# Performance work log

Hardware: AMD Instinct MI355X
Metric: run time of the kernel (lower is better)

Reference implementation:

```python
import jax, jax.numpy as jnp
import numpy as np

EPS = 1e-5

def conv1x1(x, w, b):
    # x: [B,C,H,W], w: [O,C], b: [O]
    return jnp.einsum('bchw,oc->bohw', x, w) + b[None, :, None, None]

def bn_eval(x, w, b, m, v):
    inv = w / jnp.sqrt(v + EPS)
    return (x - m[None, :, None, None]) * inv[None, :, None, None] + b[None, :, None, None]

def setup_inputs() -> dict:
    key = jax.random.key(0)
    ks = jax.random.split(key, 32)
    B, Fg, Fl, Fi, H, W = 4, 128, 128, 64, 64, 64
    d = {}
    d['g'] = jax.random.normal(ks[0], (B, Fg, H, W), jnp.float32)
    d['x'] = jax.random.normal(ks[1], (B, Fl, H, W), jnp.float32)
    d['wg_w'] = jax.random.normal(ks[2], (Fi, Fg), jnp.float32) * 0.1
    d['wg_b'] = jax.random.normal(ks[3], (Fi,), jnp.float32) * 0.1
    d['bng_w'] = jax.random.uniform(ks[4], (Fi,), jnp.float32)
    d['bng_b'] = jax.random.normal(ks[5], (Fi,), jnp.float32) * 0.1
    d['bng_m'] = jax.random.normal(ks[6], (Fi,), jnp.float32) * 0.1
    d['bng_v'] = jax.random.uniform(ks[7], (Fi,), jnp.float32) + 0.5
    d['wx_w'] = jax.random.normal(ks[8], (Fi, Fl), jnp.float32) * 0.1
    d['wx_b'] = jax.random.normal(ks[9], (Fi,), jnp.float32) * 0.1
    d['bnx_w'] = jax.random.uniform(ks[10], (Fi,), jnp.float32)
    d['bnx_b'] = jax.random.normal(ks[11], (Fi,), jnp.float32) * 0.1
    d['bnx_m'] = jax.random.normal(ks[12], (Fi,), jnp.float32) * 0.1
    d['bnx_v'] = jax.random.uniform(ks[13], (Fi,), jnp.float32) + 0.5
    d['q_w'] = jax.random.normal(ks[14], (Fi // 8, Fi), jnp.float32) * 0.1
    d['q_b'] = jax.random.normal(ks[15], (Fi // 8,), jnp.float32) * 0.1
    d['k_w'] = jax.random.normal(ks[16], (Fi // 8, Fi), jnp.float32) * 0.1
    d['k_b'] = jax.random.normal(ks[17], (Fi // 8,), jnp.float32) * 0.1
    d['v_w'] = jax.random.normal(ks[18], (Fi, Fi), jnp.float32) * 0.1
    d['v_b'] = jax.random.normal(ks[19], (Fi,), jnp.float32) * 0.1
    d['sa_gamma'] = jax.random.normal(ks[20], (1,), jnp.float32)
    d['psi_w'] = jax.random.normal(ks[21], (1, Fi), jnp.float32) * 0.1
    d['psi_b'] = jax.random.normal(ks[22], (1,), jnp.float32) * 0.1
    d['bnp_w'] = jax.random.uniform(ks[23], (1,), jnp.float32)
    d['bnp_b'] = jax.random.normal(ks[24], (1,), jnp.float32) * 0.1
    d['bnp_m'] = jax.random.normal(ks[25], (1,), jnp.float32) * 0.1
    d['bnp_v'] = jax.random.uniform(ks[26], (1,), jnp.float32) + 0.5
    return d

def reference(g, x, wg_w, wg_b, bng_w, bng_b, bng_m, bng_v,
              wx_w, wx_b, bnx_w, bnx_b, bnx_m, bnx_v,
              q_w, q_b, k_w, k_b, v_w, v_b, sa_gamma,
              psi_w, psi_b, bnp_w, bnp_b, bnp_m, bnp_v):
    g1 = bn_eval(conv1x1(g, wg_w, wg_b), bng_w, bng_b, bng_m, bng_v)
    x1 = bn_eval(conv1x1(x, wx_w, wx_b), bnx_w, bnx_b, bnx_m, bnx_v)
    c = jax.nn.relu(g1 + x1)  # [B, Fi, H, W]
    B, C, H, W = c.shape
    N = H * W
    q = conv1x1(c, q_w, q_b).reshape(B, -1, N)  # [B, Fi/8, N]
    k = conv1x1(c, k_w, k_b).reshape(B, -1, N)
    v = conv1x1(c, v_w, v_b).reshape(B, C, N)
    energy = jnp.einsum('bcn,bcm->bnm', q, k)    # [B, N, N]
    attn = jax.nn.softmax(energy, axis=-1)
    sa_out = jnp.einsum('bcm,bnm->bcn', v, attn).reshape(B, C, H, W)
    attended = sa_gamma[0] * sa_out + c
    psi = jax.nn.sigmoid(bn_eval(conv1x1(attended, psi_w, psi_b), bnp_w, bnp_b, bnp_m, bnp_v))
    return x * psi
```

## Files before the change

### kernel.cpp

```cpp
#include <hip/hip_runtime.h>
#include <hip/hip_bf16.h>


typedef short bf16x8 __attribute__((ext_vector_type(8)));
typedef unsigned short u16x8 __attribute__((ext_vector_type(8)));
typedef unsigned short u16x4 __attribute__((ext_vector_type(4)));
typedef float f32x4 __attribute__((ext_vector_type(4)));

__device__ __forceinline__ unsigned short f2b(float f) {
  unsigned u = __builtin_bit_cast(unsigned, f);
  u = (u + 0x7FFFu + ((u >> 16) & 1u)) >> 16;
  return (unsigned short)u;
}

#define EPSV 1e-5f

#define WCAT_OFF   0u
#define WQKV_OFF   32768u
#define BIASC_OFF  44032u
#define BIASQ_OFF  44288u
#define PSIW_OFF   44608u
#define SCAL_OFF   44864u
#define C_OFF      45056u
#define Q_OFF      (C_OFF + 4194304u)
#define K_OFF      (Q_OFF + 262144u)
#define V_OFF      (K_OFF + 262144u)
#define OPART_OFF  (V_OFF + 2097152u)
#define ML_OFF     (OPART_OFF + 16777216u)

__global__ __launch_bounds__(256) void prep_kernel(
    const float* __restrict__ wg_w, const float* __restrict__ wg_b,
    const float* __restrict__ bng_w, const float* __restrict__ bng_b,
    const float* __restrict__ bng_m, const float* __restrict__ bng_v,
    const float* __restrict__ wx_w, const float* __restrict__ wx_b,
    const float* __restrict__ bnx_w, const float* __restrict__ bnx_b,
    const float* __restrict__ bnx_m, const float* __restrict__ bnx_v,
    const float* __restrict__ q_w, const float* __restrict__ q_b,
    const float* __restrict__ k_w, const float* __restrict__ k_b,
    const float* __restrict__ v_w, const float* __restrict__ v_b,
    const float* __restrict__ psi_w, const float* __restrict__ psi_b,
    const float* __restrict__ bnp_w, const float* __restrict__ bnp_b,
    const float* __restrict__ bnp_m, const float* __restrict__ bnp_v,
    const float* __restrict__ sa_gamma,
    unsigned short* __restrict__ Wcat, unsigned short* __restrict__ Wqkv,
    float* __restrict__ bias_c, float* __restrict__ bias_q,
    float* __restrict__ psi_w2, float* __restrict__ scal)
{
  const int t = threadIdx.x;
  const int bid = blockIdx.x;
  if (bid < 16) {
    int o = bid * 4 + (t >> 6);
    int k = (t & 63) * 4;
    float inv;
    const float* src;
    if (k < 128) {
      inv = bng_w[o] * rsqrtf(bng_v[o] + EPSV);
      src = wg_w + o * 128 + k;
    } else {
      inv = bnx_w[o] * rsqrtf(bnx_v[o] + EPSV);
      src = wx_w + o * 128 + (k - 128);
    }
    float4 wv = *(const float4*)src;
    u16x4 pk;
    pk[0] = f2b(wv.x * inv); pk[1] = f2b(wv.y * inv);
    pk[2] = f2b(wv.z * inv); pk[3] = f2b(wv.w * inv);
    *(u16x4*)(Wcat + o * 256 + k) = pk;
    return;
  }
  for (int idx = t; idx < 80 * 64; idx += 256) {
    int r = idx >> 6, k = idx & 63;
    float wv;
    if (r < 8)       wv = q_w[r * 64 + k];
    else if (r < 16) wv = k_w[(r - 8) * 64 + k];
    else             wv = v_w[(r - 16) * 64 + k];
    Wqkv[idx] = f2b(wv);
  }
  if (t < 64) {
    int o = t;
    float invg = bng_w[o] * rsqrtf(bng_v[o] + EPSV);
    float invx = bnx_w[o] * rsqrtf(bnx_v[o] + EPSV);
    bias_c[o] = (wg_b[o] - bng_m[o]) * invg + bng_b[o]
              + (wx_b[o] - bnx_m[o]) * invx + bnx_b[o];
    float invp = bnp_w[0] * rsqrtf(bnp_v[0] + EPSV);
    psi_w2[o] = psi_w[o] * invp;
  }
  if (t < 80)
    bias_q[t] = (t < 8) ? q_b[t] : (t < 16 ? k_b[t - 8] : v_b[t - 16]);
  if (t == 0) {
    float invp = bnp_w[0] * rsqrtf(bnp_v[0] + EPSV);
    scal[0] = sa_gamma[0];
    scal[1] = (psi_b[0] - bnp_m[0]) * invp + bnp_b[0];
  }
}

__global__ __launch_bounds__(256) void conv_qkv_kernel(
    const float* __restrict__ g, const float* __restrict__ x,
    const unsigned short* __restrict__ Wcat, const unsigned short* __restrict__ Wqkv,
    const float* __restrict__ bias_c, const float* __restrict__ bias_q,
    float* __restrict__ c_out, unsigned short* __restrict__ Qb,
    unsigned short* __restrict__ Kb, unsigned short* __restrict__ Vb)
{
  __shared__ __attribute__((aligned(16))) unsigned short xt[32][264];
  __shared__ __attribute__((aligned(16))) unsigned short clds[32][72];

  const int t = threadIdx.x;
  const int bid = blockIdx.x;
  const int b = bid >> 7;
  const int n0 = (bid & 127) << 5;

  {
    const int col4 = t & 7;
    const int rowg = t >> 3;
    float4 v[8];
    #pragma unroll
    for (int rr = 0; rr < 8; ++rr) {
      int row = rowg * 8 + rr;
      const float* src = (row < 128)
          ? (g + ((size_t)(b * 128 + row)) * 4096 + n0 + col4 * 4)
          : (x + ((size_t)(b * 128 + (row - 128))) * 4096 + n0 + col4 * 4);
      v[rr] = *(const float4*)src;
    }
    #pragma unroll
    for (int j = 0; j < 4; ++j) {
      u16x8 pk;
      #pragma unroll
      for (int rr = 0; rr < 8; ++rr)
        pk[rr] = f2b(((const float*)&v[rr])[j]);
      *(u16x8*)(&xt[col4 * 4 + j][rowg * 8]) = pk;
    }
  }
  __syncthreads();

  const int l = t & 63, w = t >> 6;
  const int l15 = l & 15, lg = l >> 4;
  f32x4 zf = {0.f, 0.f, 0.f, 0.f};

  f32x4 acc[2];
  acc[0] = acc[1] = zf;
  const int orow = w * 16 + l15;
  #pragma unroll
  for (int ks = 0; ks < 8; ++ks) {
    bf16x8 af = *(const bf16x8*)(Wcat + orow * 256 + ks * 32 + lg * 8);
    #pragma unroll
    for (int ns = 0; ns < 2; ++ns) {
      bf16x8 bfv = *(const bf16x8*)(&xt[ns * 16 + l15][ks * 32 + lg * 8]);
      acc[ns] = __builtin_amdgcn_mfma_f32_16x16x32_bf16(af, bfv, acc[ns], 0, 0, 0);
    }
  }
  #pragma unroll
  for (int r = 0; r < 4; ++r) {
    int o = w * 16 + lg * 4 + r;
    float bc = bias_c[o];
    #pragma unroll
    for (int ns = 0; ns < 2; ++ns) {
      float cv = fmaxf(acc[ns][r] + bc, 0.f);
      int n = ns * 16 + l15;
      c_out[((size_t)(b * 64 + o)) * 4096 + n0 + n] = cv;
      clds[n][o] = f2b(cv);
    }
  }
  __syncthreads();

  #pragma unroll
  for (int i = 0; i < 3; ++i) {
    int tau = w + 4 * i;
    if (tau >= 10) break;
    int t5 = tau % 5, ns = tau / 5;
    f32x4 a2 = zf;
    #pragma unroll
    for (int kk = 0; kk < 2; ++kk) {
      bf16x8 af = *(const bf16x8*)(Wqkv + (t5 * 16 + l15) * 64 + kk * 32 + lg * 8);
      bf16x8 bfv = *(const bf16x8*)(&clds[ns * 16 + l15][kk * 32 + lg * 8]);
      a2 = __builtin_amdgcn_mfma_f32_16x16x32_bf16(af, bfv, a2, 0, 0, 0);
    }
    #pragma unroll
    for (int r = 0; r < 4; ++r) {
      int row = t5 * 16 + lg * 4 + r;
      int ngl = n0 + ns * 16 + l15;
      float val = a2[r] + bias_q[row];
      if (t5 == 0) {
        if (row < 8) Qb[(((size_t)b << 12) + ngl) * 8 + row] = f2b(val);
        else         Kb[(((size_t)b << 12) + ngl) * 8 + (row - 8)] = f2b(val);
      } else {
        int vch = (t5 - 1) * 16 + lg * 4 + r;
        Vb[((size_t)(b * 64 + vch)) * 4096 + ngl] = f2b(val);
      }
    }
  }
}

__global__ __launch_bounds__(256) void attn_partial_kernel(
    const unsigned short* __restrict__ Qb, const unsigned short* __restrict__ Kb,
    const unsigned short* __restrict__ Vb,
    float* __restrict__ Opart, float* __restrict__ ml)
{
  __shared__ __attribute__((aligned(16))) unsigned short klds[64][8];
  __shared__ __attribute__((aligned(16))) unsigned short vlds[64][72];
  __shared__ __attribute__((aligned(16))) unsigned short plds[4][16][72];

  const int t = threadIdx.x;
  const int bid = blockIdx.x;
  const int qt = bid & 63;
  const int b = (bid >> 6) & 3;
  const int ci = bid >> 8;
  const int n0 = qt << 6;
  const int l = t & 63, w = t >> 6;
  const int l15 = l & 15, lg = l >> 4;

  bf16x8 qf = {0, 0, 0, 0, 0, 0, 0, 0};
  if (lg == 0)
    qf = *(const bf16x8*)(Qb + (((size_t)b << 12) + n0 + w * 16 + l15) * 8);

  f32x4 zf = {0.f, 0.f, 0.f, 0.f};
  f32x4 O[4];
  O[0] = O[1] = O[2] = O[3] = zf;
  float m_run[4] = {-INFINITY, -INFINITY, -INFINITY, -INFINITY};
  float l_run[4] = {0.f, 0.f, 0.f, 0.f};

  const int m_lo = ci << 10, m_hi = (ci + 1) << 10;
  for (int m0 = m_lo; m0 < m_hi; m0 += 64) {
    if (t < 64)
      *(int4*)(&klds[t][0]) = *(const int4*)(Kb + (((size_t)b << 12) + m0 + t) * 8);
    #pragma unroll
    for (int i = 0; i < 2; ++i) {
      int ci2 = t + 256 * i;
      int row = ci2 >> 3, off = ci2 & 7;
      *(int4*)(&vlds[row][off * 8]) =
          *(const int4*)(Vb + ((size_t)(b * 64 + row)) * 4096 + m0 + off * 8);
    }
    __syncthreads();

    f32x4 e[4];
    #pragma unroll
    for (int mt = 0; mt < 4; ++mt) {
      bf16x8 kf = *(const bf16x8*)(&klds[mt * 16 + l15][0]);
      e[mt] = __builtin_amdgcn_mfma_f32_16x16x32_bf16(qf, kf, zf, 0, 0, 0);
    }

    #pragma unroll
    for (int r = 0; r < 4; ++r) {
      float vm = fmaxf(fmaxf(e[0][r], e[1][r]), fmaxf(e[2][r], e[3][r]));
      vm = fmaxf(vm, __shfl_xor(vm, 1));
      vm = fmaxf(vm, __shfl_xor(vm, 2));
      vm = fmaxf(vm, __shfl_xor(vm, 4));
      vm = fmaxf(vm, __shfl_xor(vm, 8));
      float nm = fmaxf(m_run[r], vm);
      float sc = __expf(m_run[r] - nm);
      float s = 0.f;
      #pragma unroll
      for (int mt = 0; mt < 4; ++mt) {
        float p = __expf(e[mt][r] - nm);
        e[mt][r] = p;
        s += p;
      }
      s += __shfl_xor(s, 1);
      s += __shfl_xor(s, 2);
      s += __shfl_xor(s, 4);
      s += __shfl_xor(s, 8);
      l_run[r] = l_run[r] * sc + s;
      m_run[r] = nm;
      #pragma unroll
      for (int mt = 0; mt < 4; ++mt)
        plds[w][lg * 4 + r][mt * 16 + l15] = f2b(e[mt][r]);
      #pragma unroll
      for (int ct = 0; ct < 4; ++ct) O[ct][r] *= sc;
    }

    #pragma unroll
    for (int ct = 0; ct < 4; ++ct) {
      #pragma unroll
      for (int kk = 0; kk < 2; ++kk) {
        bf16x8 pa = *(const bf16x8*)(&plds[w][l15][kk * 32 + lg * 8]);
        bf16x8 vb = *(const bf16x8*)(&vlds[ct * 16 + l15][kk * 32 + lg * 8]);
        O[ct] = __builtin_amdgcn_mfma_f32_16x16x32_bf16(pa, vb, O[ct], 0, 0, 0);
      }
    }
    __syncthreads();
  }

  const size_t pb = ((size_t)(ci * 4 + b)) << 12;
  #pragma unroll
  for (int ct = 0; ct < 4; ++ct) {
    int ch = ct * 16 + l15;
    #pragma unroll
    for (int r = 0; r < 4; ++r) {
      int qg = n0 + w * 16 + lg * 4 + r;
      Opart[(pb + qg) * 64 + ch] = O[ct][r];
    }
  }
  if (l15 == 0) {
    #pragma unroll
    for (int r = 0; r < 4; ++r) {
      int qg = n0 + w * 16 + lg * 4 + r;
      float2 mv;
      mv.x = m_run[r]; mv.y = l_run[r];
      *(float2*)(ml + (pb + qg) * 2) = mv;
    }
  }
}

__global__ __launch_bounds__(256) void combine_kernel(
    const float* __restrict__ Opart, const float* __restrict__ ml,
    const float* __restrict__ c_in, const float* __restrict__ xin,
    const float* __restrict__ psi_w2, const float* __restrict__ scal,
    float* __restrict__ out)
{
  __shared__ __attribute__((aligned(16))) float c_lds[64][68];
  __shared__ float psi_lds[64];

  const int t = threadIdx.x;
  const int bid = blockIdx.x;
  const int b = bid >> 6;
  const int n0 = (bid & 63) << 6;

  #pragma unroll
  for (int i = 0; i < 4; ++i) {
    int idx = t + 256 * i;
    int ch = idx >> 4, c4 = idx & 15;
    float4 cv = *(const float4*)(c_in + ((size_t)(b * 64 + ch)) * 4096 + n0 + c4 * 4);
    *(float4*)(&c_lds[ch][c4 * 4]) = cv;
  }
  __syncthreads();

  const int q = t >> 2, cg = t & 3;
  const int qg = n0 + q;

  float m[4], li[4];
  float M = -INFINITY;
  #pragma unroll
  for (int ci = 0; ci < 4; ++ci) {
    float2 v = *(const float2*)(ml + ((((size_t)(ci * 4 + b)) << 12) + qg) * 2);
    m[ci] = v.x; li[ci] = v.y;
    M = fmaxf(M, v.x);
  }
  float L = 0.f, wgt[4];
  #pragma unroll
  for (int ci = 0; ci < 4; ++ci) {
    wgt[ci] = __expf(m[ci] - M);
    L += wgt[ci] * li[ci];
  }
  float4 o4[4];
  o4[0] = o4[1] = o4[2] = o4[3] = make_float4(0.f, 0.f, 0.f, 0.f);
  #pragma unroll
  for (int ci = 0; ci < 4; ++ci) {
    const float* base = Opart + ((((size_t)(ci * 4 + b)) << 12) + qg) * 64 + cg * 16;
    float wv = wgt[ci];
    #pragma unroll
    for (int k = 0; k < 4; ++k) {
      float4 p = *(const float4*)(base + k * 4);
      o4[k].x += wv * p.x; o4[k].y += wv * p.y;
      o4[k].z += wv * p.z; o4[k].w += wv * p.w;
    }
  }
  const float invL = 1.f / L;
  const float gamma = scal[0], psi_c = scal[1];
  float ps = 0.f;
  #pragma unroll
  for (int k = 0; k < 4; ++k) {
    const float* op = (const float*)&o4[k];
    #pragma unroll
    for (int jj = 0; jj < 4; ++jj) {
      int ch = cg * 16 + k * 4 + jj;
      ps += psi_w2[ch] * (gamma * (op[jj] * invL) + c_lds[ch][q]);
    }
  }
  ps += __shfl_xor(ps, 1);
  ps += __shfl_xor(ps, 2);
  if (cg == 0)
    psi_lds[q] = 1.f / (1.f + __expf(-(ps + psi_c)));
  __syncthreads();

  #pragma unroll
  for (int i = 0; i < 8; ++i) {
    int idx = t + 256 * i;
    int f = idx >> 4, c4 = idx & 15;
    size_t off = ((size_t)(b * 128 + f)) * 4096 + n0 + c4 * 4;
    float4 xv = *(const float4*)(xin + off);
    float4 ov;
    ov.x = xv.x * psi_lds[c4 * 4 + 0];
    ov.y = xv.y * psi_lds[c4 * 4 + 1];
    ov.z = xv.z * psi_lds[c4 * 4 + 2];
    ov.w = xv.w * psi_lds[c4 * 4 + 3];
    *(float4*)(out + off) = ov;
  }
}

extern "C" void kernel_launch(void* const* d_in, const int* in_sizes, int n_in,
                              void* d_out, int out_size, void* d_ws, size_t ws_size,
                              hipStream_t stream) {
  (void)in_sizes; (void)n_in; (void)out_size; (void)ws_size;
  const float* g     = (const float*)d_in[0];
  const float* x     = (const float*)d_in[1];
  const float* wg_w  = (const float*)d_in[2];
  const float* wg_b  = (const float*)d_in[3];
  const float* bng_w = (const float*)d_in[4];
  const float* bng_b = (const float*)d_in[5];
  const float* bng_m = (const float*)d_in[6];
  const float* bng_v = (const float*)d_in[7];
  const float* wx_w  = (const float*)d_in[8];
  const float* wx_b  = (const float*)d_in[9];
  const float* bnx_w = (const float*)d_in[10];
  const float* bnx_b = (const float*)d_in[11];
  const float* bnx_m = (const float*)d_in[12];
  const float* bnx_v = (const float*)d_in[13];
  const float* q_w   = (const float*)d_in[14];
  const float* q_b   = (const float*)d_in[15];
  const float* k_w   = (const float*)d_in[16];
  const float* k_b   = (const float*)d_in[17];
  const float* v_w   = (const float*)d_in[18];
  const float* v_b   = (const float*)d_in[19];
  const float* sa_g  = (const float*)d_in[20];
  const float* psi_w = (const float*)d_in[21];
  const float* psi_b = (const float*)d_in[22];
  const float* bnp_w = (const float*)d_in[23];
  const float* bnp_b = (const float*)d_in[24];
  const float* bnp_m = (const float*)d_in[25];
  const float* bnp_v = (const float*)d_in[26];
  float* out = (float*)d_out;

  char* ws = (char*)d_ws;
  unsigned short* Wcat = (unsigned short*)(ws + WCAT_OFF);
  unsigned short* Wqkv = (unsigned short*)(ws + WQKV_OFF);
  float* bias_c = (float*)(ws + BIASC_OFF);
  float* bias_q = (float*)(ws + BIASQ_OFF);
  float* psiw2  = (float*)(ws + PSIW_OFF);
  float* scal   = (float*)(ws + SCAL_OFF);
  float* c_buf  = (float*)(ws + C_OFF);
  unsigned short* Qb = (unsigned short*)(ws + Q_OFF);
  unsigned short* Kb = (unsigned short*)(ws + K_OFF);
  unsigned short* Vb = (unsigned short*)(ws + V_OFF);
  float* Opart = (float*)(ws + OPART_OFF);
  float* mlb   = (float*)(ws + ML_OFF);

  hipLaunchKernelGGL(prep_kernel, dim3(17), dim3(256), 0, stream,
                     wg_w, wg_b, bng_w, bng_b, bng_m, bng_v,
                     wx_w, wx_b, bnx_w, bnx_b, bnx_m, bnx_v,
                     q_w, q_b, k_w, k_b, v_w, v_b,
                     psi_w, psi_b, bnp_w, bnp_b, bnp_m, bnp_v, sa_g,
                     Wcat, Wqkv, bias_c, bias_q, psiw2, scal);

  hipLaunchKernelGGL(conv_qkv_kernel, dim3(512), dim3(256), 0, stream,
                     g, x, Wcat, Wqkv, bias_c, bias_q, c_buf, Qb, Kb, Vb);

  hipLaunchKernelGGL(attn_partial_kernel, dim3(1024), dim3(256), 0, stream,
                     Qb, Kb, Vb, Opart, mlb);

  hipLaunchKernelGGL(combine_kernel, dim3(256), dim3(256), 0, stream,
                     Opart, mlb, c_buf, x, psiw2, scal, out);
}
```

Measured before the change: 188.9 us.

## Fuse prep into conv kernel and combine into attention via last-block counter

Weight folding (BN scale and bias) moves into the conv kernel, so the prep launch goes away. The combine step moves into the attention kernel: the last of 8 key-split blocks per query tile, found with an atomic counter, does the reduction. The key dimension is split 8 ways instead of 4, giving twice as many blocks. The c buffer and the O partials are stored in bf16 instead of fp32, and V is staged through LDS so it can be written with coalesced stores. This cuts launch count and memory traffic, at the cost of redundant per-block weight conversion, lower intermediate precision, and a counter reset that relies on the previous kernel's ordering.

```diff
diff --git a/kernel.cpp b/kernel.cpp
--- a/kernel.cpp
+++ b/kernel.cpp
@@ -7,28 +7,25 @@
 typedef unsigned short u16x4 __attribute__((ext_vector_type(4)));
 typedef float f32x4 __attribute__((ext_vector_type(4)));
 
-__device__ __forceinline__ unsigned short f2b(float f) {
-  unsigned u = __builtin_bit_cast(unsigned, f);
-  u = (u + 0x7FFFu + ((u >> 16) & 1u)) >> 16;
-  return (unsigned short)u;
+__device__ __forceinline__ unsigned short f2b16(float f) {
+  return __builtin_bit_cast(unsigned short, __float2bfloat16(f));
 }
+__device__ __forceinline__ float b2f(unsigned short u) {
+  return __bfloat162float(__builtin_bit_cast(__hip_bfloat16, u));
+}
 
 #define EPSV 1e-5f
 
-#define WCAT_OFF   0u
-#define WQKV_OFF   32768u
-#define BIASC_OFF  44032u
-#define BIASQ_OFF  44288u
-#define PSIW_OFF   44608u
-#define SCAL_OFF   44864u
-#define C_OFF      45056u
-#define Q_OFF      (C_OFF + 4194304u)
+#define C_OFF      0u
+#define Q_OFF      (C_OFF + 2097152u)
 #define K_OFF      (Q_OFF + 262144u)
 #define V_OFF      (K_OFF + 262144u)
 #define OPART_OFF  (V_OFF + 2097152u)
 #define ML_OFF     (OPART_OFF + 16777216u)
-
-__global__ __launch_bounds__(256) void prep_kernel(
+#define CNT_OFF    (ML_OFF + 1048576u)
+
+__global__ __launch_bounds__(256) void conv_fused_kernel(
+    const float* __restrict__ g, const float* __restrict__ x,
     const float* __restrict__ wg_w, const float* __restrict__ wg_b,
     const float* __restrict__ bng_w, const float* __restrict__ bng_b,
     const float* __restrict__ bng_m, const float* __restrict__ bng_v,
@@ -38,75 +35,20 @@
     const float* __restrict__ q_w, const float* __restrict__ q_b,
     const float* __restrict__ k_w, const float* __restrict__ k_b,
     const float* __restrict__ v_w, const float* __restrict__ v_b,
-    const float* __restrict__ psi_w, const float* __restrict__ psi_b,
-    const float* __restrict__ bnp_w, const float* __restrict__ bnp_b,
-    const float* __restrict__ bnp_m, const float* __restrict__ bnp_v,
-    const float* __restrict__ sa_gamma,
-    unsigned short* __restrict__ Wcat, unsigned short* __restrict__ Wqkv,
-    float* __restrict__ bias_c, float* __restrict__ bias_q,
-    float* __restrict__ psi_w2, float* __restrict__ scal)
-{
-  const int t = threadIdx.x;
-  const int bid = blockIdx.x;
-  if (bid < 16) {
-    int o = bid * 4 + (t >> 6);
-    int k = (t & 63) * 4;
-    float inv;
-    const float* src;
-    if (k < 128) {
-      inv = bng_w[o] * rsqrtf(bng_v[o] + EPSV);
-      src = wg_w + o * 128 + k;
-    } else {
-      inv = bnx_w[o] * rsqrtf(bnx_v[o] + EPSV);
-      src = wx_w + o * 128 + (k - 128);
-    }
-    float4 wv = *(const float4*)src;
-    u16x4 pk;
-    pk[0] = f2b(wv.x * inv); pk[1] = f2b(wv.y * inv);
-    pk[2] = f2b(wv.z * inv); pk[3] = f2b(wv.w * inv);
-    *(u16x4*)(Wcat + o * 256 + k) = pk;
-    return;
-  }
-  for (int idx = t; idx < 80 * 64; idx += 256) {
-    int r = idx >> 6, k = idx & 63;
-    float wv;
-    if (r < 8)       wv = q_w[r * 64 + k];
-    else if (r < 16) wv = k_w[(r - 8) * 64 + k];
-    else             wv = v_w[(r - 16) * 64 + k];
-    Wqkv[idx] = f2b(wv);
-  }
-  if (t < 64) {
-    int o = t;
-    float invg = bng_w[o] * rsqrtf(bng_v[o] + EPSV);
-    float invx = bnx_w[o] * rsqrtf(bnx_v[o] + EPSV);
-    bias_c[o] = (wg_b[o] - bng_m[o]) * invg + bng_b[o]
-              + (wx_b[o] - bnx_m[o]) * invx + bnx_b[o];
-    float invp = bnp_w[0] * rsqrtf(bnp_v[0] + EPSV);
-    psi_w2[o] = psi_w[o] * invp;
-  }
-  if (t < 80)
-    bias_q[t] = (t < 8) ? q_b[t] : (t < 16 ? k_b[t - 8] : v_b[t - 16]);
-  if (t == 0) {
-    float invp = bnp_w[0] * rsqrtf(bnp_v[0] + EPSV);
-    scal[0] = sa_gamma[0];
-    scal[1] = (psi_b[0] - bnp_m[0]) * invp + bnp_b[0];
-  }
-}
-
-__global__ __launch_bounds__(256) void conv_qkv_kernel(
-    const float* __restrict__ g, const float* __restrict__ x,
-    const unsigned short* __restrict__ Wcat, const unsigned short* __restrict__ Wqkv,
-    const float* __restrict__ bias_c, const float* __restrict__ bias_q,
-    float* __restrict__ c_out, unsigned short* __restrict__ Qb,
-    unsigned short* __restrict__ Kb, unsigned short* __restrict__ Vb)
+    unsigned short* __restrict__ cb, unsigned short* __restrict__ Qb,
+    unsigned short* __restrict__ Kb, unsigned short* __restrict__ Vb,
+    int* __restrict__ cnt)
 {
   __shared__ __attribute__((aligned(16))) unsigned short xt[32][264];
   __shared__ __attribute__((aligned(16))) unsigned short clds[32][72];
+  __shared__ __attribute__((aligned(16))) unsigned short vstage[64][36];
 
   const int t = threadIdx.x;
   const int bid = blockIdx.x;
   const int b = bid >> 7;
   const int n0 = (bid & 127) << 5;
+
+  if (bid == 0) cnt[t] = 0;
 
   {
     const int col4 = t & 7;
@@ -125,38 +67,60 @@
       u16x8 pk;
       #pragma unroll
       for (int rr = 0; rr < 8; ++rr)
-        pk[rr] = f2b(((const float*)&v[rr])[j]);
+        pk[rr] = f2b16(((const float*)&v[rr])[j]);
       *(u16x8*)(&xt[col4 * 4 + j][rowg * 8]) = pk;
     }
   }
-  __syncthreads();
 
   const int l = t & 63, w = t >> 6;
   const int l15 = l & 15, lg = l >> 4;
   f32x4 zf = {0.f, 0.f, 0.f, 0.f};
 
+  const int orow = w * 16 + l15;
+  const float invg = bng_w[orow] * rsqrtf(bng_v[orow] + EPSV);
+  const float invx = bnx_w[orow] * rsqrtf(bnx_v[orow] + EPSV);
+  bf16x8 afrag[8];
+  #pragma unroll
+  for (int ks = 0; ks < 8; ++ks) {
+    int k = ks * 32 + lg * 8;
+    const float* wp;
+    float sc;
+    if (k < 128) { wp = wg_w + orow * 128 + k;        sc = invg; }
+    else         { wp = wx_w + orow * 128 + (k - 128); sc = invx; }
+    float4 w0 = *(const float4*)wp;
+    float4 w1 = *(const float4*)(wp + 4);
+    u16x8 pk;
+    pk[0] = f2b16(w0.x * sc); pk[1] = f2b16(w0.y * sc);
+    pk[2] = f2b16(w0.z * sc); pk[3] = f2b16(w0.w * sc);
+    pk[4] = f2b16(w1.x * sc); pk[5] = f2b16(w1.y * sc);
+    pk[6] = f2b16(w1.z * sc); pk[7] = f2b16(w1.w * sc);
+    afrag[ks] = __builtin_bit_cast(bf16x8, pk);
+  }
+  __syncthreads();
+
   f32x4 acc[2];
   acc[0] = acc[1] = zf;
-  const int orow = w * 16 + l15;
   #pragma unroll
   for (int ks = 0; ks < 8; ++ks) {
-    bf16x8 af = *(const bf16x8*)(Wcat + orow * 256 + ks * 32 + lg * 8);
     #pragma unroll
     for (int ns = 0; ns < 2; ++ns) {
       bf16x8 bfv = *(const bf16x8*)(&xt[ns * 16 + l15][ks * 32 + lg * 8]);
-      acc[ns] = __builtin_amdgcn_mfma_f32_16x16x32_bf16(af, bfv, acc[ns], 0, 0, 0);
+      acc[ns] = __builtin_amdgcn_mfma_f32_16x16x32_bf16(afrag[ks], bfv, acc[ns], 0, 0, 0);
     }
   }
   #pragma unroll
   for (int r = 0; r < 4; ++r) {
     int o = w * 16 + lg * 4 + r;
-    float bc = bias_c[o];
+    float ig = bng_w[o] * rsqrtf(bng_v[o] + EPSV);
+    float ix = bnx_w[o] * rsqrtf(bnx_v[o] + EPSV);
+    float bc = (wg_b[o] - bng_m[o]) * ig + bng_b[o]
+             + (wx_b[o] - bnx_m[o]) * ix + bnx_b[o];
     #pragma unroll
     for (int ns = 0; ns < 2; ++ns) {
       float cv = fmaxf(acc[ns][r] + bc, 0.f);
-      int n = ns * 16 + l15;
-      c_out[((size_t)(b * 64 + o)) * 4096 + n0 + n] = cv;
-      clds[n][o] = f2b(cv);
+      unsigned short cv16 = f2b16(cv);
+      cb[((size_t)(b * 64 + o)) * 4096 + n0 + ns * 16 + l15] = cv16;
+      clds[ns * 16 + l15][o] = cv16;
     }
   }
   __syncthreads();
@@ -166,37 +130,75 @@
     int tau = w + 4 * i;
     if (tau >= 10) break;
     int t5 = tau % 5, ns = tau / 5;
+    int wrow = t5 * 16 + l15;
     f32x4 a2 = zf;
     #pragma unroll
     for (int kk = 0; kk < 2; ++kk) {
-      bf16x8 af = *(const bf16x8*)(Wqkv + (t5 * 16 + l15) * 64 + kk * 32 + lg * 8);
-      bf16x8 bfv = *(const bf16x8*)(&clds[ns * 16 + l15][kk * 32 + lg * 8]);
-      a2 = __builtin_amdgcn_mfma_f32_16x16x32_bf16(af, bfv, a2, 0, 0, 0);
-    }
-    #pragma unroll
-    for (int r = 0; r < 4; ++r) {
-      int row = t5 * 16 + lg * 4 + r;
-      int ngl = n0 + ns * 16 + l15;
-      float val = a2[r] + bias_q[row];
-      if (t5 == 0) {
-        if (row < 8) Qb[(((size_t)b << 12) + ngl) * 8 + row] = f2b(val);
-        else         Kb[(((size_t)b << 12) + ngl) * 8 + (row - 8)] = f2b(val);
-      } else {
+      int k = kk * 32 + lg * 8;
+      const float* wp = (wrow < 8)  ? (q_w + wrow * 64 + k)
+                      : (wrow < 16) ? (k_w + (wrow - 8) * 64 + k)
+                                    : (v_w + (wrow - 16) * 64 + k);
+      float4 w0 = *(const float4*)wp;
+      float4 w1 = *(const float4*)(wp + 4);
+      u16x8 pk;
+      pk[0] = f2b16(w0.x); pk[1] = f2b16(w0.y);
+      pk[2] = f2b16(w0.z); pk[3] = f2b16(w0.w);
+      pk[4] = f2b16(w1.x); pk[5] = f2b16(w1.y);
+      pk[6] = f2b16(w1.z); pk[7] = f2b16(w1.w);
+      bf16x8 bfv = *(const bf16x8*)(&clds[ns * 16 + l15][k]);
+      a2 = __builtin_amdgcn_mfma_f32_16x16x32_bf16(
+          __builtin_bit_cast(bf16x8, pk), bfv, a2, 0, 0, 0);
+    }
+    int ngl = n0 + ns * 16 + l15;
+    if (t5 == 0) {
+      u16x4 pk;
+      #pragma unroll
+      for (int r = 0; r < 4; ++r) {
+        int row = lg * 4 + r;
+        float bq = (row < 8) ? q_b[row] : k_b[row - 8];
+        pk[r] = f2b16(a2[r] + bq);
+      }
+      if (lg < 2)
+        *(u16x4*)(Qb + (((size_t)b << 12) + ngl) * 8 + lg * 4) = pk;
+      else
+        *(u16x4*)(Kb + (((size_t)b << 12) + ngl) * 8 + (lg - 2) * 4) = pk;
+    } else {
+      #pragma unroll
+      for (int r = 0; r < 4; ++r) {
         int vch = (t5 - 1) * 16 + lg * 4 + r;
-        Vb[((size_t)(b * 64 + vch)) * 4096 + ngl] = f2b(val);
+        vstage[vch][ns * 16 + l15] = f2b16(a2[r] + v_b[vch]);
       }
     }
   }
+  __syncthreads();
+
+  #pragma unroll
+  for (int i = 0; i < 2; ++i) {
+    int idx = t + 256 * i;
+    int row = idx >> 3, seg = idx & 7;
+    u16x4 pv = *(const u16x4*)(&vstage[row][seg * 4]);
+    *(u16x4*)(Vb + ((size_t)(b * 64 + row)) * 4096 + n0 + seg * 4) = pv;
+  }
 }
 
-__global__ __launch_bounds__(256) void attn_partial_kernel(
+__global__ __launch_bounds__(256) void attn_fused_kernel(
     const unsigned short* __restrict__ Qb, const unsigned short* __restrict__ Kb,
-    const unsigned short* __restrict__ Vb,
-    float* __restrict__ Opart, float* __restrict__ ml)
+    const unsigned short* __restrict__ Vb, const unsigned short* __restrict__ cb,
+    const float* __restrict__ xin,
+    const float* __restrict__ psi_w, const float* __restrict__ psi_b,
+    const float* __restrict__ bnp_w, const float* __restrict__ bnp_b,
+    const float* __restrict__ bnp_m, const float* __restrict__ bnp_v,
+    const float* __restrict__ sa_gamma,
+    unsigned short* __restrict__ Opart, float* __restrict__ ml,
+    int* __restrict__ cnt, float* __restrict__ out)
 {
-  __shared__ __attribute__((aligned(16))) unsigned short klds[64][8];
-  __shared__ __attribute__((aligned(16))) unsigned short vlds[64][72];
-  __shared__ __attribute__((aligned(16))) unsigned short plds[4][16][72];
+  __shared__ __attribute__((aligned(16))) char smem[19456];
+  __shared__ int is_last;
+  auto klds = (unsigned short(*)[8])smem;
+  auto vlds = (unsigned short(*)[72])(smem + 1024);
+  auto plds = (unsigned short(*)[16][72])(smem + 10240);
+  auto ml_lds = (float2(*)[8])smem;
+  float* psi_lds = (float*)(smem + 4096);
 
   const int t = threadIdx.x;
   const int bid = blockIdx.x;
@@ -217,7 +219,7 @@
   float m_run[4] = {-INFINITY, -INFINITY, -INFINITY, -INFINITY};
   float l_run[4] = {0.f, 0.f, 0.f, 0.f};
 
-  const int m_lo = ci << 10, m_hi = (ci + 1) << 10;
+  const int m_lo = ci << 9, m_hi = (ci + 1) << 9;
   for (int m0 = m_lo; m0 < m_hi; m0 += 64) {
     if (t < 64)
       *(int4*)(&klds[t][0]) = *(const int4*)(Kb + (((size_t)b << 12) + m0 + t) * 8);
@@ -261,7 +263,7 @@
       m_run[r] = nm;
       #pragma unroll
       for (int mt = 0; mt < 4; ++mt)
-        plds[w][lg * 4 + r][mt * 16 + l15] = f2b(e[mt][r]);
+        plds[w][lg * 4 + r][mt * 16 + l15] = f2b16(e[mt][r]);
       #pragma unroll
       for (int ct = 0; ct < 4; ++ct) O[ct][r] *= sc;
     }
@@ -285,7 +287,7 @@
     #pragma unroll
     for (int r = 0; r < 4; ++r) {
       int qg = n0 + w * 16 + lg * 4 + r;
-      Opart[(pb + qg) * 64 + ch] = O[ct][r];
+      Opart[(pb + qg) * 64 + ch] = f2b16(O[ct][r]);
     }
   }
   if (l15 == 0) {
@@ -297,72 +299,61 @@
       *(float2*)(ml + (pb + qg) * 2) = mv;
     }
   }
-}
-
-__global__ __launch_bounds__(256) void combine_kernel(
-    const float* __restrict__ Opart, const float* __restrict__ ml,
-    const float* __restrict__ c_in, const float* __restrict__ xin,
-    const float* __restrict__ psi_w2, const float* __restrict__ scal,
-    float* __restrict__ out)
-{
-  __shared__ __attribute__((aligned(16))) float c_lds[64][68];
-  __shared__ float psi_lds[64];
-
-  const int t = threadIdx.x;
-  const int bid = blockIdx.x;
-  const int b = bid >> 6;
-  const int n0 = (bid & 63) << 6;
-
-  #pragma unroll
-  for (int i = 0; i < 4; ++i) {
+
+  __threadfence();
+  __syncthreads();
+  if (t == 0)
+    is_last = (atomicAdd(&cnt[b * 64 + qt], 1) == 7);
+  __syncthreads();
+  if (!is_last) return;
+  __threadfence();
+
+  #pragma unroll
+  for (int i = 0; i < 2; ++i) {
     int idx = t + 256 * i;
-    int ch = idx >> 4, c4 = idx & 15;
-    float4 cv = *(const float4*)(c_in + ((size_t)(b * 64 + ch)) * 4096 + n0 + c4 * 4);
-    *(float4*)(&c_lds[ch][c4 * 4]) = cv;
-  }
-  __syncthreads();
+    int cj = idx >> 6, q = idx & 63;
+    ml_lds[q][cj] = *(const float2*)(ml + ((((size_t)(cj * 4 + b)) << 12) + n0 + q) * 2);
+  }
+  __syncthreads();
+
+  const float invp = bnp_w[0] * rsqrtf(bnp_v[0] + EPSV);
+  const float psi_c = (psi_b[0] - bnp_m[0]) * invp + bnp_b[0];
+  const float gamma = sa_gamma[0];
 
   const int q = t >> 2, cg = t & 3;
   const int qg = n0 + q;
 
-  float m[4], li[4];
   float M = -INFINITY;
   #pragma unroll
-  for (int ci = 0; ci < 4; ++ci) {
-    float2 v = *(const float2*)(ml + ((((size_t)(ci * 4 + b)) << 12) + qg) * 2);
-    m[ci] = v.x; li[ci] = v.y;
-    M = fmaxf(M, v.x);
-  }
-  float L = 0.f, wgt[4];
-  #pragma unroll
-  for (int ci = 0; ci < 4; ++ci) {
-    wgt[ci] = __expf(m[ci] - M);
-    L += wgt[ci] * li[ci];
-  }
-  float4 o4[4];
-  o4[0] = o4[1] = o4[2] = o4[3] = make_float4(0.f, 0.f, 0.f, 0.f);
-  #pragma unroll
-  for (int ci = 0; ci < 4; ++ci) {
-    const float* base = Opart + ((((size_t)(ci * 4 + b)) << 12) + qg) * 64 + cg * 16;
-    float wv = wgt[ci];
-    #pragma unroll
-    for (int k = 0; k < 4; ++k) {
-      float4 p = *(const float4*)(base + k * 4);
-      o4[k].x += wv * p.x; o4[k].y += wv * p.y;
-      o4[k].z += wv * p.z; o4[k].w += wv * p.w;
+  for (int cj = 0; cj < 8; ++cj) M = fmaxf(M, ml_lds[q][cj].x);
+  float L = 0.f, wgt[8];
+  #pragma unroll
+  for (int cj = 0; cj < 8; ++cj) {
+    wgt[cj] = __expf(ml_lds[q][cj].x - M);
+    L += wgt[cj] * ml_lds[q][cj].y;
+  }
+  float osum[16];
+  #pragma unroll
+  for (int k = 0; k < 16; ++k) osum[k] = 0.f;
+  #pragma unroll
+  for (int cj = 0; cj < 8; ++cj) {
+    const unsigned short* base =
+        Opart + ((((size_t)(cj * 4 + b)) << 12) + qg) * 64 + cg * 16;
+    float wv = wgt[cj];
+    #pragma unroll
+    for (int s4 = 0; s4 < 4; ++s4) {
+      u16x4 p = *(const u16x4*)(base + s4 * 4);
+      #pragma unroll
+      for (int j = 0; j < 4; ++j) osum[s4 * 4 + j] += wv * b2f(p[j]);
     }
   }
   const float invL = 1.f / L;
-  const float gamma = scal[0], psi_c = scal[1];
   float ps = 0.f;
   #pragma unroll
-  for (int k = 0; k < 4; ++k) {
-    const float* op = (const float*)&o4[k];
-    #pragma unroll
-    for (int jj = 0; jj < 4; ++jj) {
-      int ch = cg * 16 + k * 4 + jj;
-      ps += psi_w2[ch] * (gamma * (op[jj] * invL) + c_lds[ch][q]);
-    }
+  for (int k = 0; k < 16; ++k) {
+    int ch = cg * 16 + k;
+    float cv = b2f(cb[((size_t)(b * 64 + ch)) * 4096 + qg]);
+    ps += (psi_w[ch] * invp) * (gamma * (osum[k] * invL) + cv);
   }
   ps += __shfl_xor(ps, 1);
   ps += __shfl_xor(ps, 2);
@@ -419,32 +410,22 @@
   float* out = (float*)d_out;
 
   char* ws = (char*)d_ws;
-  unsigned short* Wcat = (unsigned short*)(ws + WCAT_OFF);
-  unsigned short* Wqkv = (unsigned short*)(ws + WQKV_OFF);
-  float* bias_c = (float*)(ws + BIASC_OFF);
-  float* bias_q = (float*)(ws + BIASQ_OFF);
-  float* psiw2  = (float*)(ws + PSIW_OFF);
-  float* scal   = (float*)(ws + SCAL_OFF);
-  float* c_buf  = (float*)(ws + C_OFF);
+  unsigned short* cb = (unsigned short*)(ws + C_OFF);
   unsigned short* Qb = (unsigned short*)(ws + Q_OFF);
   unsigned short* Kb = (unsigned short*)(ws + K_OFF);
   unsigned short* Vb = (unsigned short*)(ws + V_OFF);
-  float* Opart = (float*)(ws + OPART_OFF);
-  float* mlb   = (float*)(ws + ML_OFF);
-
-  hipLaunchKernelGGL(prep_kernel, dim3(17), dim3(256), 0, stream,
-                     wg_w, wg_b, bng_w, bng_b, bng_m, bng_v,
+  unsigned short* Opart = (unsigned short*)(ws + OPART_OFF);
+  float* mlb = (float*)(ws + ML_OFF);
+  int* cnt   = (int*)(ws + CNT_OFF);
+
+  hipLaunchKernelGGL(conv_fused_kernel, dim3(512), dim3(256), 0, stream,
+                     g, x, wg_w, wg_b, bng_w, bng_b, bng_m, bng_v,
                      wx_w, wx_b, bnx_w, bnx_b, bnx_m, bnx_v,
                      q_w, q_b, k_w, k_b, v_w, v_b,
+                     cb, Qb, Kb, Vb, cnt);
+
+  hipLaunchKernelGGL(attn_fused_kernel, dim3(2048), dim3(256), 0, stream,
+                     Qb, Kb, Vb, cb, x,
                      psi_w, psi_b, bnp_w, bnp_b, bnp_m, bnp_v, sa_g,
-                     Wcat, Wqkv, bias_c, bias_q, psiw2, scal);
-
-  hipLaunchKernelGGL(conv_qkv_kernel, dim3(512), dim3(256), 0, stream,
-                     g, x, Wcat, Wqkv, bias_c, bias_q, c_buf, Qb, Kb, Vb);
-
-  hipLaunchKernelGGL(attn_partial_kernel, dim3(1024), dim3(256), 0, stream,
-                     Qb, Kb, Vb, Opart, mlb);
-
-  hipLaunchKernelGGL(combine_kernel, dim3(256), dim3(256), 0, stream,
-                     Opart, mlb, c_buf, x, psiw2, scal, out);
+                     Opart, mlb, cnt, out);
 }
```

Result: slower. 419.8 us (+122.2%).
